# Performance work log

Hardware: AMD Instinct MI355X
Metric: run time of the kernel (lower is better)

Reference implementation:

```python
import jax, jax.numpy as jnp
import numpy as np
from jax import lax

B, S, D_IN, D_STATE, D_OUT, N_HEADS = 4, 2048, 2048, 2048, 2048, 16
H = D_STATE // N_HEADS  # 128


def setup_inputs() -> dict:
    key = jax.random.key(0)
    k1, k2, k3, k4, k5 = jax.random.split(key, 5)
    x = jax.random.normal(k1, (B, S, D_IN), dtype=jnp.float32)
    Wi = jax.random.normal(k2, (D_IN, D_STATE), dtype=jnp.float32) * (D_IN ** -0.5)
    b = jax.random.normal(k3, (D_STATE,), dtype=jnp.float32) * 0.01
    # state_weight is init'd with normal_ in torch; scale down for numerical sanity
    state_w = jax.random.normal(k4, (N_HEADS, H, H), dtype=jnp.float32) * (H ** -0.5)
    Wo = jax.random.normal(k5, (D_STATE, D_OUT), dtype=jnp.float32) * (D_STATE ** -0.5)
    input_state = jnp.zeros((B, D_STATE), dtype=jnp.float32)
    return {"x": x, "input_state": input_state, "Wi": Wi, "b": b,
            "state_w": state_w, "Wo": Wo}


def _rnn_forward(x, input_state, Wi, b, state_w, Wo):
    # input projection: [B,S,D_IN] -> [B,S,N,H]
    xp = (jnp.einsum('bsd,de->bse', x, Wi) + b).reshape(B, S, N_HEADS, H)
    h0 = input_state.reshape(B, N_HEADS, H)

    def step(h, xt):  # h: [B,N,H], xt: [B,N,H]
        h = jnp.tanh(jnp.einsum('bnh,nhk->bnk', h, state_w) + xt)
        return h, h

    _, hs = lax.scan(step, h0, jnp.moveaxis(xp, 1, 0))  # hs: [S,B,N,H]
    hs = jnp.moveaxis(hs, 0, 1)                         # [B,S,N,H]
    output_state = hs[:, -1].reshape(B, D_STATE)        # [B, state_size]
    out = jnp.einsum('bsd,de->bse', hs.reshape(B, S, D_STATE), Wo)
    return out, output_state


def reference(x, input_state, Wi, b, state_w, Wo):
    return _rnn_forward(x, input_state, Wi, b, state_w, Wo)
```

## Files before the change

kernel.cpp:

```cpp
#include <hip/hip_runtime.h>
#include <hip/hip_bf16.h>

#define B_ 4
#define S_ 2048
#define DIN 2048
#define DST 2048
#define DOUT 2048
#define NH 16
#define HH 128
#define M_ (B_ * S_)
#define OUT_OFF ((size_t)M_ * DOUT)

typedef __attribute__((ext_vector_type(8))) __bf16 bf16x8;
typedef __attribute__((ext_vector_type(4))) float f32x4;
typedef __attribute__((ext_vector_type(2))) _Float16 f16x2;

__device__ __forceinline__ unsigned short f2bf(float f) {
    unsigned int u = __float_as_uint(f);
    unsigned int r = u + 0x7FFFu + ((u >> 16) & 1u);
    return (unsigned short)(r >> 16);
}
__device__ __forceinline__ unsigned pk16(_Float16 a, _Float16 b) {
    return (unsigned)__builtin_bit_cast(unsigned short, a) |
           ((unsigned)__builtin_bit_cast(unsigned short, b) << 16);
}

__device__ __forceinline__ float fdot2(f16x2 a, f16x2 b, float c) {
#if __has_builtin(__builtin_amdgcn_fdot2)
    return __builtin_amdgcn_fdot2(a, b, c, false);
#else
    return fmaf((float)a.x, (float)b.x, fmaf((float)a.y, (float)b.y, c));
#endif
}
__device__ __forceinline__ float fdu(unsigned h, unsigned w, float c) {
    return fdot2(__builtin_bit_cast(f16x2, h), __builtin_bit_cast(f16x2, w), c);
}

__device__ __forceinline__ void gload_lds16(const void* g, void* l) {
    __builtin_amdgcn_global_load_lds(
        (const __attribute__((address_space(1))) void*)g,
        (__attribute__((address_space(3))) void*)l, 16, 0, 0);
}

__global__ __launch_bounds__(256) void k_cast_bf16(
    const float* __restrict__ in, unsigned short* __restrict__ out, int n8) {
    int i = blockIdx.x * 256 + threadIdx.x;
    if (i >= n8) return;
    const float4* p = ((const float4*)in) + (size_t)i * 2;
    float4 a = p[0], b = p[1];
    ushort4 r0, r1;
    r0.x = f2bf(a.x); r0.y = f2bf(a.y); r0.z = f2bf(a.z); r0.w = f2bf(a.w);
    r1.x = f2bf(b.x); r1.y = f2bf(b.y); r1.z = f2bf(b.z); r1.w = f2bf(b.w);
    ushort4* o = ((ushort4*)out) + (size_t)i * 2;
    o[0] = r0; o[1] = r1;
}

__global__ __launch_bounds__(256) void k_transpose_bf16(
    const float* __restrict__ in, unsigned short* __restrict__ out, int K, int N) {
    __shared__ float tile[64][65];
    int k0 = blockIdx.y * 64, n0 = blockIdx.x * 64;
    int tr  = threadIdx.x >> 4;
    int tc4 = (threadIdx.x & 15) * 4;
#pragma unroll
    for (int p = 0; p < 4; ++p) {
        int r = tr + p * 16;
        float4 v = *(const float4*)&in[(size_t)(k0 + r) * N + n0 + tc4];
        tile[r][tc4 + 0] = v.x; tile[r][tc4 + 1] = v.y;
        tile[r][tc4 + 2] = v.z; tile[r][tc4 + 3] = v.w;
    }
    __syncthreads();
#pragma unroll
    for (int p = 0; p < 4; ++p) {
        int n = tr + p * 16;
        ushort4 o;
        o.x = f2bf(tile[tc4 + 0][n]); o.y = f2bf(tile[tc4 + 1][n]);
        o.z = f2bf(tile[tc4 + 2][n]); o.w = f2bf(tile[tc4 + 3][n]);
        *(ushort4*)&out[(size_t)(n0 + n) * K + k0 + tc4] = o;
    }
}

__global__ __launch_bounds__(256, 2) void k_gemm_bt(
    const unsigned short* __restrict__ A,
    const unsigned short* __restrict__ Bt,
    void* __restrict__ C,
    const float* __restrict__ bias,
    int M, int N, int K, int outF16) {
    __shared__ unsigned short As[128 * 64];
    __shared__ unsigned short Bs[128 * 64];
    const int tid  = threadIdx.x;
    const int lane = tid & 63;
    const int wid  = tid >> 6;
    const int wr = wid >> 1, wc = wid & 1;
    const int row0 = blockIdx.y * 128, col0 = blockIdx.x * 128;

    f32x4 acc[4][4];
#pragma unroll
    for (int m = 0; m < 4; ++m)
#pragma unroll
        for (int n = 0; n < 4; ++n) acc[m][n] = (f32x4)(0.f);

    const char* Abase = (const char*)(A + (size_t)row0 * K);
    const char* Bbase = (const char*)(Bt + (size_t)col0 * K);

    int srow[4], skb[4];
#pragma unroll
    for (int i = 0; i < 4; ++i) {
        unsigned o = (unsigned)(i * 256 + tid) * 16u;
        unsigned l = o ^ (((o >> 7) & 7u) << 4);
        srow[i] = (int)(l >> 7);
        skb[i]  = (int)(l & 127u);
    }

    for (int kt = 0; kt < K; kt += 64) {
#pragma unroll
        for (int i = 0; i < 4; ++i) {
            unsigned o = (unsigned)(i * 256 + tid) * 16u;
            gload_lds16(Abase + (size_t)srow[i] * (K * 2) + (size_t)kt * 2 + skb[i],
                        (char*)As + o);
            gload_lds16(Bbase + (size_t)srow[i] * (K * 2) + (size_t)kt * 2 + skb[i],
                        (char*)Bs + o);
        }
        asm volatile("s_waitcnt vmcnt(0)" ::: "memory");
        __syncthreads();
#pragma unroll
        for (int ks = 0; ks < 2; ++ks) {
            bf16x8 af[4], bfr[4];
#pragma unroll
            for (int m = 0; m < 4; ++m) {
                int row = wr * 64 + m * 16 + (lane & 15);
                unsigned o = (unsigned)(row * 128 + ks * 64 + ((lane >> 4) * 16));
                o ^= ((unsigned)(row & 7) << 4);
                af[m] = *(const bf16x8*)((const char*)As + o);
            }
#pragma unroll
            for (int n = 0; n < 4; ++n) {
                int col = wc * 64 + n * 16 + (lane & 15);
                unsigned o = (unsigned)(col * 128 + ks * 64 + ((lane >> 4) * 16));
                o ^= ((unsigned)(col & 7) << 4);
                bfr[n] = *(const bf16x8*)((const char*)Bs + o);
            }
#pragma unroll
            for (int m = 0; m < 4; ++m)
#pragma unroll
                for (int n = 0; n < 4; ++n)
                    acc[m][n] = __builtin_amdgcn_mfma_f32_16x16x32_bf16(
                        af[m], bfr[n], acc[m][n], 0, 0, 0);
        }
        __syncthreads();
    }

#pragma unroll
    for (int n = 0; n < 4; ++n) {
        int gcol = col0 + wc * 64 + n * 16 + (lane & 15);
        float bv = outF16 ? bias[gcol] : 0.f;
#pragma unroll
        for (int m = 0; m < 4; ++m) {
            int growb = row0 + wr * 64 + m * 16 + ((lane >> 4) * 4);
#pragma unroll
            for (int r = 0; r < 4; ++r) {
                float v = acc[m][n][r] + bv;
                size_t off = (size_t)(growb + r) * N + gcol;
                if (outF16)
                    ((unsigned short*)C)[off] =
                        __builtin_bit_cast(unsigned short, (_Float16)v);
                else
                    ((float*)C)[off] = v;
            }
        }
    }
}

__global__ __attribute__((amdgpu_flat_work_group_size(64, 64),
                          amdgpu_waves_per_eu(1, 1))) void k_scan(
    const unsigned short* __restrict__ xpf,
    const float* __restrict__ h0,
    const float* __restrict__ sw,
    unsigned short* __restrict__ hsb,
    float* __restrict__ out_state) {
    __shared__ __align__(16) unsigned hb[64];
    __shared__ __align__(16) unsigned wlA[2048];
    __shared__ __align__(16) unsigned wlB[2048];
    const int l = threadIdx.x;
    const int bb = blockIdx.x >> 4;
    const int nn = blockIdx.x & 15;
    const int c0 = l * 2;

    const float* wb = sw + (size_t)nn * HH * HH;

    f16x2 wA[32], wB[32];
#pragma unroll
    for (int j = 0; j < 32; ++j) {
        float2 rA = *(const float2*)&wb[(size_t)(2 * j) * HH + c0];
        float2 rB = *(const float2*)&wb[(size_t)(2 * j + 1) * HH + c0];
        wA[j] = f16x2{(_Float16)rA.x, (_Float16)rB.x};
        wB[j] = f16x2{(_Float16)rA.y, (_Float16)rB.y};
    }
#pragma unroll
    for (int j = 0; j < 32; ++j) {
        float2 rA = *(const float2*)&wb[(size_t)(64 + 2 * j) * HH + c0];
        float2 rB = *(const float2*)&wb[(size_t)(64 + 2 * j + 1) * HH + c0];
        unsigned off = (unsigned)(l * 128) +
                       (((unsigned)(j >> 2) * 16u) ^ ((unsigned)(l & 7) << 4)) +
                       (unsigned)(j & 3) * 4u;
        *(unsigned*)((char*)wlA + off) = pk16((_Float16)rA.x, (_Float16)rB.x);
        *(unsigned*)((char*)wlB + off) = pk16((_Float16)rA.y, (_Float16)rB.y);
    }

    {
        float2 h2 = *(const float2*)&h0[bb * DST + nn * HH + c0];
        hb[l] = pk16((_Float16)h2.x, (_Float16)h2.y);
    }

    const unsigned* xrow = (const unsigned*)(xpf + (size_t)bb * S_ * DST + nn * HH) + l;
    unsigned* hrow = (unsigned*)(hsb + (size_t)bb * S_ * DST + nn * HH) + l;
    float* osp = out_state + bb * DST + nn * HH + c0;

    unsigned x0 = xrow[0], x1 = xrow[1024], x2 = xrow[2048], x3 = xrow[3072];

    const uint4* hp = (const uint4*)hb;

    for (int t = 0; t < S_; ++t) {
        int tpf = (t + 4 < S_) ? t + 4 : S_ - 1;
        unsigned x4 = xrow[(size_t)tpf * 1024];

        float a0 = 0.f, a1 = 0.f, a2 = 0.f, a3 = 0.f;
        float b0 = 0.f, b1 = 0.f, b2 = 0.f, b3 = 0.f;

#pragma unroll
        for (int k = 0; k < 8; ++k) {
            uint4 H = hp[k];
            a0 = fdu(H.x, __builtin_bit_cast(unsigned, wA[4 * k + 0]), a0);
            b0 = fdu(H.x, __builtin_bit_cast(unsigned, wB[4 * k + 0]), b0);
            a1 = fdu(H.y, __builtin_bit_cast(unsigned, wA[4 * k + 1]), a1);
            b1 = fdu(H.y, __builtin_bit_cast(unsigned, wB[4 * k + 1]), b1);
            a2 = fdu(H.z, __builtin_bit_cast(unsigned, wA[4 * k + 2]), a2);
            b2 = fdu(H.z, __builtin_bit_cast(unsigned, wB[4 * k + 2]), b2);
            a3 = fdu(H.w, __builtin_bit_cast(unsigned, wA[4 * k + 3]), a3);
            b3 = fdu(H.w, __builtin_bit_cast(unsigned, wB[4 * k + 3]), b3);
        }
#pragma unroll
        for (int k = 0; k < 8; ++k) {
            uint4 H = hp[8 + k];
            unsigned off = (unsigned)(l * 128) +
                           (((unsigned)k * 16u) ^ ((unsigned)(l & 7) << 4));
            uint4 WAc = *(const uint4*)((const char*)wlA + off);
            uint4 WBc = *(const uint4*)((const char*)wlB + off);
            a0 = fdu(H.x, WAc.x, a0); b0 = fdu(H.x, WBc.x, b0);
            a1 = fdu(H.y, WAc.y, a1); b1 = fdu(H.y, WBc.y, b1);
            a2 = fdu(H.z, WAc.z, a2); b2 = fdu(H.z, WBc.z, b2);
            a3 = fdu(H.w, WAc.w, a3); b3 = fdu(H.w, WBc.w, b3);
        }

        f16x2 xv = __builtin_bit_cast(f16x2, x0);
        float s0 = ((a0 + a1) + (a2 + a3)) + (float)xv.x;
        float s1 = ((b0 + b1) + (b2 + b3)) + (float)xv.y;
        float e0 = __builtin_amdgcn_exp2f(s0 * 2.885390081777927f);
        float e1 = __builtin_amdgcn_exp2f(s1 * 2.885390081777927f);
        float th0 = fmaf(-2.f, __builtin_amdgcn_rcpf(e0 + 1.f), 1.f);
        float th1 = fmaf(-2.f, __builtin_amdgcn_rcpf(e1 + 1.f), 1.f);

        hb[l] = pk16((_Float16)th0, (_Float16)th1);
        hrow[(size_t)t * (DST / 2)] = (unsigned)f2bf(th0) | ((unsigned)f2bf(th1) << 16);
        if (t == S_ - 1) { osp[0] = th0; osp[1] = th1; }

        x0 = x1; x1 = x2; x2 = x3; x3 = x4;
    }
}

extern "C" void kernel_launch(void* const* d_in, const int* in_sizes, int n_in,
                              void* d_out, int out_size, void* d_ws, size_t ws_size,
                              hipStream_t stream) {
    const float* x    = (const float*)d_in[0];
    const float* h0   = (const float*)d_in[1];
    const float* Wi   = (const float*)d_in[2];
    const float* bias = (const float*)d_in[3];
    const float* sw   = (const float*)d_in[4];
    const float* Wo   = (const float*)d_in[5];
    float* out = (float*)d_out;

    char* ws = (char*)d_ws;
    unsigned short* xb  = (unsigned short*)ws;
    unsigned short* wit = (unsigned short*)(ws + 33554432);
    unsigned short* wot = (unsigned short*)(ws + 41943040);
    unsigned short* xpf = (unsigned short*)(ws + 50331648);

    k_cast_bf16<<<8192, 256, 0, stream>>>(x, xb, (M_ * DIN) / 8);
    dim3 tg(32, 32);
    k_transpose_bf16<<<tg, 256, 0, stream>>>(Wi, wit, DIN, DST);
    k_transpose_bf16<<<tg, 256, 0, stream>>>(Wo, wot, DST, DOUT);
    dim3 g1(DST / 128, M_ / 128);
    k_gemm_bt<<<g1, 256, 0, stream>>>(xb, wit, xpf, bias, M_, DST, DIN, 1);
    k_scan<<<64, 64, 0, stream>>>(xpf, h0, sw, xb, out + OUT_OFF);
    dim3 g2(DOUT / 128, M_ / 128);
    k_gemm_bt<<<g2, 256, 0, stream>>>(xb, wot, out, nullptr, M_, DOUT, DST, 0);
}
```

Baseline: 1.019 ms.

## Fuse x bf16 cast into GEMM1 loads and hold scan weights in registers

```diff
diff --git a/kernel.cpp b/kernel.cpp
--- a/kernel.cpp
+++ b/kernel.cpp
@@ -42,19 +42,6 @@
         (__attribute__((address_space(3))) void*)l, 16, 0, 0);
 }
 
-__global__ __launch_bounds__(256) void k_cast_bf16(
-    const float* __restrict__ in, unsigned short* __restrict__ out, int n8) {
-    int i = blockIdx.x * 256 + threadIdx.x;
-    if (i >= n8) return;
-    const float4* p = ((const float4*)in) + (size_t)i * 2;
-    float4 a = p[0], b = p[1];
-    ushort4 r0, r1;
-    r0.x = f2bf(a.x); r0.y = f2bf(a.y); r0.z = f2bf(a.z); r0.w = f2bf(a.w);
-    r1.x = f2bf(b.x); r1.y = f2bf(b.y); r1.z = f2bf(b.z); r1.w = f2bf(b.w);
-    ushort4* o = ((ushort4*)out) + (size_t)i * 2;
-    o[0] = r0; o[1] = r1;
-}
-
 __global__ __launch_bounds__(256) void k_transpose_bf16(
     const float* __restrict__ in, unsigned short* __restrict__ out, int K, int N) {
     __shared__ float tile[64][65];
@@ -79,12 +66,11 @@
     }
 }
 
-__global__ __launch_bounds__(256, 2) void k_gemm_bt(
-    const unsigned short* __restrict__ A,
+__global__ __launch_bounds__(256, 2) void k_gemm1(
+    const float* __restrict__ x,
     const unsigned short* __restrict__ Bt,
-    void* __restrict__ C,
-    const float* __restrict__ bias,
-    int M, int N, int K, int outF16) {
+    unsigned short* __restrict__ xpf,
+    const float* __restrict__ bias) {
     __shared__ unsigned short As[128 * 64];
     __shared__ unsigned short Bs[128 * 64];
     const int tid  = threadIdx.x;
@@ -99,8 +85,8 @@
 #pragma unroll
         for (int n = 0; n < 4; ++n) acc[m][n] = (f32x4)(0.f);
 
-    const char* Abase = (const char*)(A + (size_t)row0 * K);
-    const char* Bbase = (const char*)(Bt + (size_t)col0 * K);
+    const float* Ab = x + (size_t)row0 * DIN;
+    const char* Bb = (const char*)(Bt + (size_t)col0 * DIN);
 
     int srow[4], skb[4];
 #pragma unroll
@@ -111,13 +97,23 @@
         skb[i]  = (int)(l & 127u);
     }
 
-    for (int kt = 0; kt < K; kt += 64) {
+    for (int kt = 0; kt < DIN; kt += 64) {
+#pragma unroll
+        for (int i = 0; i < 8; ++i) {
+            int idx = i * 256 + tid;
+            int row = idx >> 4;
+            int cc  = (idx & 15) * 4;
+            float4 v = *(const float4*)&Ab[(size_t)row * DIN + kt + cc];
+            ushort4 u;
+            u.x = f2bf(v.x); u.y = f2bf(v.y); u.z = f2bf(v.z); u.w = f2bf(v.w);
+            unsigned byte = (unsigned)(row * 128 + cc * 2);
+            byte ^= ((unsigned)(row & 7)) << 4;
+            *(ushort4*)((char*)As + byte) = u;
+        }
 #pragma unroll
         for (int i = 0; i < 4; ++i) {
             unsigned o = (unsigned)(i * 256 + tid) * 16u;
-            gload_lds16(Abase + (size_t)srow[i] * (K * 2) + (size_t)kt * 2 + skb[i],
-                        (char*)As + o);
-            gload_lds16(Bbase + (size_t)srow[i] * (K * 2) + (size_t)kt * 2 + skb[i],
+            gload_lds16(Bb + (size_t)srow[i] * (DIN * 2) + (size_t)kt * 2 + skb[i],
                         (char*)Bs + o);
         }
         asm volatile("s_waitcnt vmcnt(0)" ::: "memory");
@@ -152,20 +148,97 @@
 #pragma unroll
     for (int n = 0; n < 4; ++n) {
         int gcol = col0 + wc * 64 + n * 16 + (lane & 15);
-        float bv = outF16 ? bias[gcol] : 0.f;
+        float bv = bias[gcol];
 #pragma unroll
         for (int m = 0; m < 4; ++m) {
             int growb = row0 + wr * 64 + m * 16 + ((lane >> 4) * 4);
 #pragma unroll
             for (int r = 0; r < 4; ++r) {
                 float v = acc[m][n][r] + bv;
-                size_t off = (size_t)(growb + r) * N + gcol;
-                if (outF16)
-                    ((unsigned short*)C)[off] =
-                        __builtin_bit_cast(unsigned short, (_Float16)v);
-                else
-                    ((float*)C)[off] = v;
-            }
+                xpf[(size_t)(growb + r) * DST + gcol] =
+                    __builtin_bit_cast(unsigned short, (_Float16)v);
+            }
+        }
+    }
+}
+
+__global__ __launch_bounds__(256, 2) void k_gemm2(
+    const unsigned short* __restrict__ A,
+    const unsigned short* __restrict__ Bt,
+    float* __restrict__ C) {
+    __shared__ unsigned short As[128 * 64];
+    __shared__ unsigned short Bs[128 * 64];
+    const int tid  = threadIdx.x;
+    const int lane = tid & 63;
+    const int wid  = tid >> 6;
+    const int wr = wid >> 1, wc = wid & 1;
+    const int row0 = blockIdx.y * 128, col0 = blockIdx.x * 128;
+
+    f32x4 acc[4][4];
+#pragma unroll
+    for (int m = 0; m < 4; ++m)
+#pragma unroll
+        for (int n = 0; n < 4; ++n) acc[m][n] = (f32x4)(0.f);
+
+    const char* Abase = (const char*)(A + (size_t)row0 * DST);
+    const char* Bbase = (const char*)(Bt + (size_t)col0 * DST);
+
+    int srow[4], skb[4];
+#pragma unroll
+    for (int i = 0; i < 4; ++i) {
+        unsigned o = (unsigned)(i * 256 + tid) * 16u;
+        unsigned l = o ^ (((o >> 7) & 7u) << 4);
+        srow[i] = (int)(l >> 7);
+        skb[i]  = (int)(l & 127u);
+    }
+
+    for (int kt = 0; kt < DST; kt += 64) {
+#pragma unroll
+        for (int i = 0; i < 4; ++i) {
+            unsigned o = (unsigned)(i * 256 + tid) * 16u;
+            gload_lds16(Abase + (size_t)srow[i] * (DST * 2) + (size_t)kt * 2 + skb[i],
+                        (char*)As + o);
+            gload_lds16(Bbase + (size_t)srow[i] * (DST * 2) + (size_t)kt * 2 + skb[i],
+                        (char*)Bs + o);
+        }
+        asm volatile("s_waitcnt vmcnt(0)" ::: "memory");
+        __syncthreads();
+#pragma unroll
+        for (int ks = 0; ks < 2; ++ks) {
+            bf16x8 af[4], bfr[4];
+#pragma unroll
+            for (int m = 0; m < 4; ++m) {
+                int row = wr * 64 + m * 16 + (lane & 15);
+                unsigned o = (unsigned)(row * 128 + ks * 64 + ((lane >> 4) * 16));
+                o ^= ((unsigned)(row & 7) << 4);
+                af[m] = *(const bf16x8*)((const char*)As + o);
+            }
+#pragma unroll
+            for (int n = 0; n < 4; ++n) {
+                int col = wc * 64 + n * 16 + (lane & 15);
+                unsigned o = (unsigned)(col * 128 + ks * 64 + ((lane >> 4) * 16));
+                o ^= ((unsigned)(col & 7) << 4);
+                bfr[n] = *(const bf16x8*)((const char*)Bs + o);
+            }
+#pragma unroll
+            for (int m = 0; m < 4; ++m)
+#pragma unroll
+                for (int n = 0; n < 4; ++n)
+                    acc[m][n] = __builtin_amdgcn_mfma_f32_16x16x32_bf16(
+                        af[m], bfr[n], acc[m][n], 0, 0, 0);
+        }
+        __syncthreads();
+    }
+
+#pragma unroll
+    for (int n = 0; n < 4; ++n) {
+        int gcol = col0 + wc * 64 + n * 16 + (lane & 15);
+#pragma unroll
+        for (int m = 0; m < 4; ++m) {
+            int growb = row0 + wr * 64 + m * 16 + ((lane >> 4) * 4);
+            float* cp = C + (size_t)growb * DOUT + gcol;
+#pragma unroll
+            for (int r = 0; r < 4; ++r) cp[(size_t)r * DOUT] = acc[m][n][r];
         }
     }
 }
@@ -178,8 +251,6 @@
     unsigned short* __restrict__ hsb,
     float* __restrict__ out_state) {
     __shared__ __align__(16) unsigned hb[64];
-    __shared__ __align__(16) unsigned wlA[2048];
-    __shared__ __align__(16) unsigned wlB[2048];
     const int l = threadIdx.x;
     const int bb = blockIdx.x >> 4;
     const int nn = blockIdx.x & 15;
@@ -187,23 +258,17 @@
 
     const float* wb = sw + (size_t)nn * HH * HH;
 
-    f16x2 wA[32], wB[32];
-#pragma unroll
-    for (int j = 0; j < 32; ++j) {
-        float2 rA = *(const float2*)&wb[(size_t)(2 * j) * HH + c0];
-        float2 rB = *(const float2*)&wb[(size_t)(2 * j + 1) * HH + c0];
-        wA[j] = f16x2{(_Float16)rA.x, (_Float16)rB.x};
-        wB[j] = f16x2{(_Float16)rA.y, (_Float16)rB.y};
-    }
-#pragma unroll
-    for (int j = 0; j < 32; ++j) {
-        float2 rA = *(const float2*)&wb[(size_t)(64 + 2 * j) * HH + c0];
-        float2 rB = *(const float2*)&wb[(size_t)(64 + 2 * j + 1) * HH + c0];
-        unsigned off = (unsigned)(l * 128) +
-                       (((unsigned)(j >> 2) * 16u) ^ ((unsigned)(l & 7) << 4)) +
-                       (unsigned)(j & 3) * 4u;
-        *(unsigned*)((char*)wlA + off) = pk16((_Float16)rA.x, (_Float16)rB.x);
-        *(unsigned*)((char*)wlB + off) = pk16((_Float16)rA.y, (_Float16)rB.y);
+    unsigned wu[128];
+#pragma unroll
+    for (int k = 0; k < 64; ++k) {
+        float2 rA = *(const float2*)&wb[(size_t)(2 * k) * HH + c0];
+        float2 rB = *(const float2*)&wb[(size_t)(2 * k + 1) * HH + c0];
+        unsigned a = pk16((_Float16)rA.x, (_Float16)rB.x);
+        unsigned b = pk16((_Float16)rA.y, (_Float16)rB.y);
+        asm volatile("" : "+v"(a));
+        asm volatile("" : "+v"(b));
+        wu[k] = a;
+        wu[64 + k] = b;
     }
 
     {
@@ -225,30 +290,13 @@
 
         float a0 = 0.f, a1 = 0.f, a2 = 0.f, a3 = 0.f;
         float b0 = 0.f, b1 = 0.f, b2 = 0.f, b3 = 0.f;
-
-#pragma unroll
-        for (int k = 0; k < 8; ++k) {
-            uint4 H = hp[k];
-            a0 = fdu(H.x, __builtin_bit_cast(unsigned, wA[4 * k + 0]), a0);
-            b0 = fdu(H.x, __builtin_bit_cast(unsigned, wB[4 * k + 0]), b0);
-            a1 = fdu(H.y, __builtin_bit_cast(unsigned, wA[4 * k + 1]), a1);
-            b1 = fdu(H.y, __builtin_bit_cast(unsigned, wB[4 * k + 1]), b1);
-            a2 = fdu(H.z, __builtin_bit_cast(unsigned, wA[4 * k + 2]), a2);
-            b2 = fdu(H.z, __builtin_bit_cast(unsigned, wB[4 * k + 2]), b2);
-            a3 = fdu(H.w, __builtin_bit_cast(unsigned, wA[4 * k + 3]), a3);
-            b3 = fdu(H.w, __builtin_bit_cast(unsigned, wB[4 * k + 3]), b3);
-        }
-#pragma unroll
-        for (int k = 0; k < 8; ++k) {
-            uint4 H = hp[8 + k];
-            unsigned off = (unsigned)(l * 128) +
-                           (((unsigned)k * 16u) ^ ((unsigned)(l & 7) << 4));
-            uint4 WAc = *(const uint4*)((const char*)wlA + off);
-            uint4 WBc = *(const uint4*)((const char*)wlB + off);
-            a0 = fdu(H.x, WAc.x, a0); b0 = fdu(H.x, WBc.x, b0);
-            a1 = fdu(H.y, WAc.y, a1); b1 = fdu(H.y, WBc.y, b1);
-            a2 = fdu(H.z, WAc.z, a2); b2 = fdu(H.z, WBc.z, b2);
-            a3 = fdu(H.w, WAc.w, a3); b3 = fdu(H.w, WBc.w, b3);
+#pragma unroll
+        for (int j = 0; j < 16; ++j) {
+            uint4 H = hp[j];
+            a0 = fdu(H.x, wu[4 * j + 0], a0); b0 = fdu(H.x, wu[64 + 4 * j + 0], b0);
+            a1 = fdu(H.y, wu[4 * j + 1], a1); b1 = fdu(H.y, wu[64 + 4 * j + 1], b1);
+            a2 = fdu(H.z, wu[4 * j + 2], a2); b2 = fdu(H.z, wu[64 + 4 * j + 2], b2);
+            a3 = fdu(H.w, wu[4 * j + 3], a3); b3 = fdu(H.w, wu[64 + 4 * j + 3], b3);
         }
 
         f16x2 xv = __builtin_bit_cast(f16x2, x0);
@@ -279,18 +327,17 @@
     float* out = (float*)d_out;
 
     char* ws = (char*)d_ws;
-    unsigned short* xb  = (unsigned short*)ws;
+    unsigned short* hsb = (unsigned short*)ws;
     unsigned short* wit = (unsigned short*)(ws + 33554432);
     unsigned short* wot = (unsigned short*)(ws + 41943040);
     unsigned short* xpf = (unsigned short*)(ws + 50331648);
 
-    k_cast_bf16<<<8192, 256, 0, stream>>>(x, xb, (M_ * DIN) / 8);
     dim3 tg(32, 32);
     k_transpose_bf16<<<tg, 256, 0, stream>>>(Wi, wit, DIN, DST);
     k_transpose_bf16<<<tg, 256, 0, stream>>>(Wo, wot, DST, DOUT);
     dim3 g1(DST / 128, M_ / 128);
-    k_gemm_bt<<<g1, 256, 0, stream>>>(xb, wit, xpf, bias, M_, DST, DIN, 1);
-    k_scan<<<64, 64, 0, stream>>>(xpf, h0, sw, xb, out + OUT_OFF);
+    k_gemm1<<<g1, 256, 0, stream>>>(x, wit, xpf, bias);
+    k_scan<<<64, 64, 0, stream>>>(xpf, h0, sw, hsb, out + OUT_OFF);
     dim3 g2(DOUT / 128, M_ / 128);
-    k_gemm_bt<<<g2, 256, 0, stream>>>(xb, wot, out, nullptr, M_, DOUT, DST, 0);
-}
+    k_gemm2<<<g2, 256, 0, stream>>>(hsb, wot, out);
+}
```

Result: slower. 1.043 ms (+2.4%).
